# Performance work log

Hardware: AMD Instinct MI355X
Metric: run time of the kernel (lower is better)

## Reference

```python
import jax, jax.numpy as jnp
import numpy as np

TAU = 0.07        # temperature from init_kwargs
EPS = 1e-8        # torch F.cosine_similarity eps
NEG_INF = -1e9    # mask fill value used by the original module


def setup_inputs() -> dict:
    key = jax.random.key(0)
    k1, k2 = jax.random.split(key)
    B, D = 4096, 512
    anchor = jax.random.normal(k1, (B, D), dtype=jnp.float32)
    positive = jax.random.normal(k2, (B, D), dtype=jnp.float32)
    return {"anchor": anchor, "positive": positive}


def reference(anchor, positive):
    B = anchor.shape[0]
    N = 2 * B
    emb = jnp.concatenate([anchor, positive], axis=0)          # (2B, D)
    # cosine similarity matrix == normalized dot products (same math as the
    # broadcasted F.cosine_similarity, without the O(N^2 D) intermediate)
    norm = jnp.maximum(jnp.linalg.norm(emb, axis=1, keepdims=True), EPS)
    z = emb / norm
    sim = jnp.matmul(z, z.T) / TAU                             # (2B, 2B)

    idx = jnp.arange(N)
    pos_idx = (idx + B) % N                                    # positive pair index
    pos_logits = sim[idx, pos_idx][:, None]                    # (2B, 1)

    # negatives: everything except self and the positive pair
    neg_mask = (
        jnp.ones((N, N), dtype=bool)
        .at[idx, idx].set(False)
        .at[idx, pos_idx].set(False)
    )
    neg_logits = jnp.where(neg_mask, sim, NEG_INF)             # (2B, 2B)

    all_logits = jnp.concatenate([pos_logits, neg_logits], axis=1)  # (2B, 2B+1)
    loss_per_sample = -pos_logits[:, 0] + jax.scipy.special.logsumexp(all_logits, axis=1)
    # every row has a positive, so valid_samples is all-True; reduction='mean'
    return loss_per_sample.mean()
```

## Files before the change

### kernel.cpp

```cpp
#include <hip/hip_runtime.h>
#include <hip/hip_bf16.h>
#include <stdint.h>


#define N_TOT   8192
#define B_HALF  4096
#define DDIM    512
#define INV_TAU 14.285714285714286f

typedef float floatx4 __attribute__((ext_vector_type(4)));

__device__ __forceinline__ void gl2lds16(const void* g, void* l) {
    __builtin_amdgcn_global_load_lds(
        (const __attribute__((address_space(1))) void*)g,
        (__attribute__((address_space(3))) void*)l, 16, 0, 0);
}

__global__ __launch_bounds__(256) void knorm(const float* __restrict__ anchor,
                                             const float* __restrict__ positive,
                                             uint8_t* __restrict__ z,
                                             float* __restrict__ row_sums,
                                             float* __restrict__ pos_sims,
                                             float* __restrict__ out) {
    const int w    = threadIdx.x >> 6;
    const int lane = threadIdx.x & 63;
    const int row  = blockIdx.x * 4 + w;
    const int prow = row + B_HALF;
    if (blockIdx.x == 0 && threadIdx.x == 0) out[0] = 0.0f;

    const float* a = anchor   + (size_t)row * DDIM;
    const float* p = positive + (size_t)row * DDIM;
    float4 a0 = ((const float4*)a)[lane];
    float4 a1 = ((const float4*)a)[lane + 64];
    float4 p0 = ((const float4*)p)[lane];
    float4 p1 = ((const float4*)p)[lane + 64];

    float ssa = a0.x*a0.x + a0.y*a0.y + a0.z*a0.z + a0.w*a0.w
              + a1.x*a1.x + a1.y*a1.y + a1.z*a1.z + a1.w*a1.w;
    float ssp = p0.x*p0.x + p0.y*p0.y + p0.z*p0.z + p0.w*p0.w
              + p1.x*p1.x + p1.y*p1.y + p1.z*p1.z + p1.w*p1.w;
    float dot = a0.x*p0.x + a0.y*p0.y + a0.z*p0.z + a0.w*p0.w
              + a1.x*p1.x + a1.y*p1.y + a1.z*p1.z + a1.w*p1.w;
    #pragma unroll
    for (int m = 1; m < 64; m <<= 1) {
        ssa += __shfl_xor(ssa, m, 64);
        ssp += __shfl_xor(ssp, m, 64);
        dot += __shfl_xor(dot, m, 64);
    }
    const float inva = 1.0f / fmaxf(sqrtf(ssa), 1e-8f);
    const float invp = 1.0f / fmaxf(sqrtf(ssp), 1e-8f);
    const float psim = dot * inva * invp * INV_TAU;
    if (lane == 0) {
        pos_sims[row]  = psim;  pos_sims[prow] = psim;
        row_sums[row]  = 0.0f;  row_sums[prow] = 0.0f;
    }

    uint32_t qa0 = __builtin_amdgcn_cvt_pk_fp8_f32(a0.x*inva, a0.y*inva, 0, 0);
    qa0          = __builtin_amdgcn_cvt_pk_fp8_f32(a0.z*inva, a0.w*inva, qa0, 1);
    uint32_t qa1 = __builtin_amdgcn_cvt_pk_fp8_f32(a1.x*inva, a1.y*inva, 0, 0);
    qa1          = __builtin_amdgcn_cvt_pk_fp8_f32(a1.z*inva, a1.w*inva, qa1, 1);
    uint32_t qp0 = __builtin_amdgcn_cvt_pk_fp8_f32(p0.x*invp, p0.y*invp, 0, 0);
    qp0          = __builtin_amdgcn_cvt_pk_fp8_f32(p0.z*invp, p0.w*invp, qp0, 1);
    uint32_t qp1 = __builtin_amdgcn_cvt_pk_fp8_f32(p1.x*invp, p1.y*invp, 0, 0);
    qp1          = __builtin_amdgcn_cvt_pk_fp8_f32(p1.z*invp, p1.w*invp, qp1, 1);
    uint32_t* za = (uint32_t*)(z + (size_t)row  * DDIM);
    uint32_t* zp = (uint32_t*)(z + (size_t)prow * DDIM);
    za[lane] = qa0; za[lane + 64] = qa1;
    zp[lane] = qp0; zp[lane + 64] = qp1;
}

__global__ __launch_bounds__(256, 4) void ksim(const uint8_t* __restrict__ z,
                                               float* __restrict__ row_sums) {
    const int bid = (int)blockIdx.x;
    int rem = (bid & 7) * 260 + (bid >> 3);
    int gr = 0, gc = 0;
    for (;;) {
        const int sz = (gr == gc) ? 36 : 64;
        if (rem < sz) break;
        rem -= sz;
        if (++gc == 8) { gr++; gc = gr; }
    }
    int rt, ct;
    if (gr == gc) {
        int i = 0;
        while (rem >= 8 - i) { rem -= 8 - i; i++; }
        rt = gr * 8 + i;
        ct = gc * 8 + i + rem;
    } else {
        rt = gr * 8 + (rem >> 3);
        ct = gc * 8 + (rem & 7);
    }
    const bool diag = (rt == ct);
    const bool posb = (ct == rt + 32);

    const int r0 = rt * 128, c0 = ct * 128;
    const int tid  = threadIdx.x;
    const int w    = tid >> 6, lane = tid & 63;
    const int quad = lane >> 4, nlo = lane & 15;
    const int wrow = (w >> 1) * 64, wcol = (w & 1) * 64;

    __shared__ __align__(16) char smem[32768];
    char* As = smem;
    char* Bs = smem + 16384;
    const char* Bbase = diag ? As : Bs;

    floatx4 acc[4][4];
    #pragma unroll
    for (int a = 0; a < 4; a++)
        #pragma unroll
        for (int b = 0; b < 4; b++) acc[a][b] = (floatx4){0.f, 0.f, 0.f, 0.f};

    const int srow = lane >> 3;
    const int p    = lane & 7;

    for (int kb = 0; kb < 4; kb++) {
        #pragma unroll
        for (int it = 0; it < 4; it++) {
            const int c  = w * 4 + it;
            const int rr = c * 8 + srow;
            const int lc = (p - rr) & 7;
            gl2lds16(z + (size_t)(r0 + rr) * DDIM + kb * 128 + lc * 16,
                     As + c * 1024);
            if (!diag)
                gl2lds16(z + (size_t)(c0 + rr) * DDIM + kb * 128 + lc * 16,
                         Bs + c * 1024);
        }
        __syncthreads();

        #pragma unroll
        for (int ks = 0; ks < 4; ks++) {
            const int g  = ks * 4 + quad;
            const int lc = g >> 1, h = g & 1;
            long af[4], bfr[4];
            #pragma unroll
            for (int mi = 0; mi < 4; mi++) {
                const int rr = wrow + mi * 16 + nlo;
                const int pc = (lc + rr) & 7;
                af[mi] = *(const long*)(As + rr * 128 + pc * 16 + h * 8);
            }
            #pragma unroll
            for (int ni = 0; ni < 4; ni++) {
                const int rr = wcol + ni * 16 + nlo;
                const int pc = (lc + rr) & 7;
                bfr[ni] = *(const long*)(Bbase + rr * 128 + pc * 16 + h * 8);
            }
            #pragma unroll
            for (int mi = 0; mi < 4; mi++)
                #pragma unroll
                for (int ni = 0; ni < 4; ni++)
                    acc[mi][ni] = __builtin_amdgcn_mfma_f32_16x16x32_fp8_fp8(
                        af[mi], bfr[ni], acc[mi][ni], 0, 0, 0);
        }
        __syncthreads();
    }

    if (diag) {
        #pragma unroll
        for (int mi = 0; mi < 4; mi++) {
            #pragma unroll
            for (int reg = 0; reg < 4; reg++) {
                const int i = r0 + wrow + mi * 16 + quad * 4 + reg;
                float rs = 0.f;
                #pragma unroll
                for (int ni = 0; ni < 4; ni++) {
                    const int j2 = c0 + wcol + ni * 16 + nlo;
                    const float e = __expf(acc[mi][ni][reg] * INV_TAU - INV_TAU);
                    rs += (j2 == i) ? 0.f : e;
                }
                rs += __shfl_xor(rs, 1, 64);
                rs += __shfl_xor(rs, 2, 64);
                rs += __shfl_xor(rs, 4, 64);
                rs += __shfl_xor(rs, 8, 64);
                if (nlo == 0) atomicAdd(&row_sums[i], rs);
            }
        }
    } else {
        float cs[4] = {0.f, 0.f, 0.f, 0.f};
        #pragma unroll
        for (int mi = 0; mi < 4; mi++) {
            #pragma unroll
            for (int reg = 0; reg < 4; reg++) {
                const int i = r0 + wrow + mi * 16 + quad * 4 + reg;
                const int ipos = i ^ B_HALF;
                float rs = 0.f;
                #pragma unroll
                for (int ni = 0; ni < 4; ni++) {
                    const int j2 = c0 + wcol + ni * 16 + nlo;
                    float e = __expf(acc[mi][ni][reg] * INV_TAU - INV_TAU);
                    if (posb && j2 == ipos) e = 0.f;
                    rs += e;
                    cs[ni] += e;
                }
                rs += __shfl_xor(rs, 1, 64);
                rs += __shfl_xor(rs, 2, 64);
                rs += __shfl_xor(rs, 4, 64);
                rs += __shfl_xor(rs, 8, 64);
                if (nlo == 0) atomicAdd(&row_sums[i], rs);
            }
        }
        #pragma unroll
        for (int ni = 0; ni < 4; ni++) {
            float c = cs[ni];
            c += __shfl_xor(c, 16, 64);
            c += __shfl_xor(c, 32, 64);
            if (quad == 0)
                atomicAdd(&row_sums[c0 + wcol + ni * 16 + nlo], c);
        }
    }
}

__global__ __launch_bounds__(256) void kfinal(const float* __restrict__ row_sums,
                                              const float* __restrict__ pos_sims,
                                              float* __restrict__ out) {
    const int r = blockIdx.x * 256 + threadIdx.x;
    const float ps = pos_sims[r];
    float v = INV_TAU + __logf(row_sums[r] + __expf(ps - INV_TAU)) - ps;
    #pragma unroll
    for (int m = 1; m < 64; m <<= 1) v += __shfl_xor(v, m, 64);
    __shared__ float wsum[4];
    if ((threadIdx.x & 63) == 0) wsum[threadIdx.x >> 6] = v;
    __syncthreads();
    if (threadIdx.x == 0)
        atomicAdd(out, (wsum[0] + wsum[1] + wsum[2] + wsum[3]) * (1.0f / (float)N_TOT));
}

extern "C" void kernel_launch(void* const* d_in, const int* in_sizes, int n_in,
                              void* d_out, int out_size, void* d_ws, size_t ws_size,
                              hipStream_t stream) {
    const float* anchor   = (const float*)d_in[0];
    const float* positive = (const float*)d_in[1];
    float* out = (float*)d_out;

    char* ws = (char*)d_ws;
    uint8_t* z        = (uint8_t*)ws;
    float*   row_sums = (float*)(ws + 4194304);
    float*   pos_sims = (float*)(ws + 4194304 + 32768);

    knorm<<<B_HALF / 4, 256, 0, stream>>>(anchor, positive, z, row_sums,
                                          pos_sims, out);
    ksim<<<2080, 256, 0, stream>>>(z, row_sums);
    kfinal<<<N_TOT / 256, 256, 0, stream>>>(row_sums, pos_sims, out);
}
```

Measured before the change: 111.0 us.

## Fuse final reduction into sim kernel via last-block counter; halve K tile

Removes the separate final-reduction kernel launch. The last ksim block to finish, found through an atomic completion counter, now computes the per-row losses and writes the mean. The K-chunk is halved from 128 to 64 bytes, cutting LDS from 32KB to 16KB per block and doubling the number of sync rounds. Wave priority is raised around the MFMA section. The cost is a serial final pass over 8192 rows done by one block, plus extra barriers per K step.

```diff
diff --git a/kernel.cpp b/kernel.cpp
--- a/kernel.cpp
+++ b/kernel.cpp
@@ -21,12 +21,12 @@
                                              uint8_t* __restrict__ z,
                                              float* __restrict__ row_sums,
                                              float* __restrict__ pos_sims,
-                                             float* __restrict__ out) {
+                                             unsigned* __restrict__ done_ctr) {
     const int w    = threadIdx.x >> 6;
     const int lane = threadIdx.x & 63;
     const int row  = blockIdx.x * 4 + w;
     const int prow = row + B_HALF;
-    if (blockIdx.x == 0 && threadIdx.x == 0) out[0] = 0.0f;
+    if (blockIdx.x == 0 && threadIdx.x == 0) *done_ctr = 0u;
 
     const float* a = anchor   + (size_t)row * DDIM;
     const float* p = positive + (size_t)row * DDIM;
@@ -69,8 +69,11 @@
     zp[lane] = qp0; zp[lane + 64] = qp1;
 }
 
-__global__ __launch_bounds__(256, 4) void ksim(const uint8_t* __restrict__ z,
-                                               float* __restrict__ row_sums) {
+__global__ __launch_bounds__(256) void ksim(const uint8_t* __restrict__ z,
+                                            float* __restrict__ row_sums,
+                                            const float* __restrict__ pos_sims,
+                                            unsigned* __restrict__ done_ctr,
+                                            float* __restrict__ out) {
     const int bid = (int)blockIdx.x;
     int rem = (bid & 7) * 260 + (bid >> 3);
     int gr = 0, gc = 0;
@@ -99,9 +102,11 @@
     const int quad = lane >> 4, nlo = lane & 15;
     const int wrow = (w >> 1) * 64, wcol = (w & 1) * 64;
 
-    __shared__ __align__(16) char smem[32768];
+    __shared__ __align__(16) char smem[16384];
+    __shared__ unsigned lastf;
+    __shared__ float fsum[4];
     char* As = smem;
-    char* Bs = smem + 16384;
+    char* Bs = smem + 8192;
     const char* Bbase = diag ? As : Bs;
 
     floatx4 acc[4][4];
@@ -110,39 +115,40 @@
         #pragma unroll
         for (int b = 0; b < 4; b++) acc[a][b] = (floatx4){0.f, 0.f, 0.f, 0.f};
 
-    const int srow = lane >> 3;
-    const int p    = lane & 7;
-
-    for (int kb = 0; kb < 4; kb++) {
-        #pragma unroll
-        for (int it = 0; it < 4; it++) {
-            const int c  = w * 4 + it;
-            const int rr = c * 8 + srow;
-            const int lc = (p - rr) & 7;
-            gl2lds16(z + (size_t)(r0 + rr) * DDIM + kb * 128 + lc * 16,
+    const int srow = lane >> 2;
+    const int p    = lane & 3;
+
+    for (int kb = 0; kb < 8; kb++) {
+        #pragma unroll
+        for (int it = 0; it < 2; it++) {
+            const int c  = w * 2 + it;
+            const int rr = c * 16 + srow;
+            const int lc = (p - rr) & 3;
+            gl2lds16(z + (size_t)(r0 + rr) * DDIM + kb * 64 + lc * 16,
                      As + c * 1024);
             if (!diag)
-                gl2lds16(z + (size_t)(c0 + rr) * DDIM + kb * 128 + lc * 16,
+                gl2lds16(z + (size_t)(c0 + rr) * DDIM + kb * 64 + lc * 16,
                          Bs + c * 1024);
         }
         __syncthreads();
 
-        #pragma unroll
-        for (int ks = 0; ks < 4; ks++) {
+        __builtin_amdgcn_s_setprio(1);
+        #pragma unroll
+        for (int ks = 0; ks < 2; ks++) {
             const int g  = ks * 4 + quad;
             const int lc = g >> 1, h = g & 1;
             long af[4], bfr[4];
             #pragma unroll
             for (int mi = 0; mi < 4; mi++) {
                 const int rr = wrow + mi * 16 + nlo;
-                const int pc = (lc + rr) & 7;
-                af[mi] = *(const long*)(As + rr * 128 + pc * 16 + h * 8);
+                const int pc = (lc + rr) & 3;
+                af[mi] = *(const long*)(As + rr * 64 + pc * 16 + h * 8);
             }
             #pragma unroll
             for (int ni = 0; ni < 4; ni++) {
                 const int rr = wcol + ni * 16 + nlo;
-                const int pc = (lc + rr) & 7;
-                bfr[ni] = *(const long*)(Bbase + rr * 128 + pc * 16 + h * 8);
+                const int pc = (lc + rr) & 3;
+                bfr[ni] = *(const long*)(Bbase + rr * 64 + pc * 16 + h * 8);
             }
             #pragma unroll
             for (int mi = 0; mi < 4; mi++)
@@ -151,6 +157,7 @@
                     acc[mi][ni] = __builtin_amdgcn_mfma_f32_16x16x32_fp8_fp8(
                         af[mi], bfr[ni], acc[mi][ni], 0, 0, 0);
         }
+        __builtin_amdgcn_s_setprio(0);
         __syncthreads();
     }
 
@@ -207,21 +214,24 @@
                 atomicAdd(&row_sums[c0 + wcol + ni * 16 + nlo], c);
         }
     }
-}
-
-__global__ __launch_bounds__(256) void kfinal(const float* __restrict__ row_sums,
-                                              const float* __restrict__ pos_sims,
-                                              float* __restrict__ out) {
-    const int r = blockIdx.x * 256 + threadIdx.x;
-    const float ps = pos_sims[r];
-    float v = INV_TAU + __logf(row_sums[r] + __expf(ps - INV_TAU)) - ps;
+
+    __threadfence();
+    __syncthreads();
+    if (tid == 0) lastf = (atomicAdd(done_ctr, 1u) == 2079u) ? 1u : 0u;
+    __syncthreads();
+    if (!lastf) return;
+    __threadfence();
+    float a = 0.f;
+    for (int i = tid; i < N_TOT; i += 256) {
+        const float ps = pos_sims[i];
+        a += INV_TAU + __logf(row_sums[i] + __expf(ps - INV_TAU)) - ps;
+    }
     #pragma unroll
-    for (int m = 1; m < 64; m <<= 1) v += __shfl_xor(v, m, 64);
-    __shared__ float wsum[4];
-    if ((threadIdx.x & 63) == 0) wsum[threadIdx.x >> 6] = v;
+    for (int m = 1; m < 64; m <<= 1) a += __shfl_xor(a, m, 64);
+    if (lane == 0) fsum[w] = a;
     __syncthreads();
-    if (threadIdx.x == 0)
-        atomicAdd(out, (wsum[0] + wsum[1] + wsum[2] + wsum[3]) * (1.0f / (float)N_TOT));
+    if (tid == 0)
+        out[0] = (fsum[0] + fsum[1] + fsum[2] + fsum[3]) * (1.0f / (float)N_TOT);
 }
 
 extern "C" void kernel_launch(void* const* d_in, const int* in_sizes, int n_in,
@@ -232,12 +242,12 @@
     float* out = (float*)d_out;
 
     char* ws = (char*)d_ws;
-    uint8_t* z        = (uint8_t*)ws;
-    float*   row_sums = (float*)(ws + 4194304);
-    float*   pos_sims = (float*)(ws + 4194304 + 32768);
+    uint8_t*  z        = (uint8_t*)ws;
+    float*    row_sums = (float*)(ws + 4194304);
+    float*    pos_sims = (float*)(ws + 4194304 + 32768);
+    unsigned* done_ctr = (unsigned*)(ws + 4194304 + 65536);
 
     knorm<<<B_HALF / 4, 256, 0, stream>>>(anchor, positive, z, row_sums,
-                                          pos_sims, out);
-    ksim<<<2080, 256, 0, stream>>>(z, row_sums);
-    kfinal<<<N_TOT / 256, 256, 0, stream>>>(row_sums, pos_sims, out);
-}
+                                          pos_sims, done_ctr);
+    ksim<<<2080, 256, 0, stream>>>(z, row_sums, pos_sims, done_ctr, out);
+}
```

New measurement: 254.3 us. 129% more time.
